# Optimization experiments

Measured on AMD Instinct MI355X. Metric: run time of the kernel, lower is better.

The kernel has to match this reference:

```python
import jax, jax.numpy as jnp
import numpy as np

M_USERS = 100000
N_ITEMS = 50000
N_NODES = M_USERS + N_ITEMS
DIM = 64
N_INTER = 1600000
BATCH = 16384
N_NEG = 40
REG = 1e-4


def setup_inputs() -> dict:
    key = jax.random.key(0)
    ks = jax.random.split(key, 12)
    xavier = lambda k, shape: jax.random.normal(k, shape, jnp.float32) * np.sqrt(2.0 / (shape[-1] + shape[-2] if len(shape) >= 2 else shape[-1] + 1))
    E = jax.random.normal(ks[0], (N_NODES, DIM), jnp.float32) * 0.1
    E2 = jax.random.normal(ks[1], (N_NODES, DIM), jnp.float32) * 0.1
    Wm = jax.random.normal(ks[2], (2, DIM, DIM), jnp.float32) * np.sqrt(1.0 / DIM)
    bm = jnp.zeros((2, DIM), jnp.float32)
    attn_W = jax.random.normal(ks[3], (DIM, DIM), jnp.float32) * np.sqrt(1.0 / DIM)
    attn_b = jnp.zeros((DIM,), jnp.float32)
    q_w = jax.random.normal(ks[4], (DIM,), jnp.float32) * np.sqrt(1.0 / DIM)
    # symmetric bipartite edge list: users in [0, M), items in [M, M+N)
    eu = jax.random.randint(ks[5], (N_INTER,), 0, M_USERS, jnp.int32)
    ei = jax.random.randint(ks[6], (N_INTER,), M_USERS, N_NODES, jnp.int32)
    edge_index = jnp.stack([jnp.concatenate([eu, ei]), jnp.concatenate([ei, eu])], axis=0)
    u = jax.random.randint(ks[7], (BATCH,), 0, M_USERS, jnp.int32)
    v = jax.random.randint(ks[8], (BATCH,), M_USERS, N_NODES, jnp.int32)
    n = jax.random.randint(ks[9], (BATCH, N_NEG), M_USERS, N_NODES, jnp.int32)
    w = jax.random.uniform(ks[10], (BATCH,), jnp.float32, 0.5, 5.0)  # ratings; only sign() used
    return {"E": E, "E2": E2, "Wm": Wm, "bm": bm, "attn_W": attn_W, "attn_b": attn_b,
            "q_w": q_w, "edge_index": edge_index, "u": u, "v": v, "n": n, "w": w}


def _lightgconv(x, src, dst, norm):
    # out[i] = sum_{(j->i)} norm_e * x[j]   (symmetric-normalized LightGCN propagate)
    msg = x[src] * norm[:, None]  # [E, D]
    return jax.ops.segment_sum(msg, dst, num_segments=N_NODES)


def _aggregate(E, E2, Wm, bm, attn_W, attn_b, q_w, edge_index):
    src, dst = edge_index[0], edge_index[1]
    deg = jax.ops.segment_sum(jnp.ones(src.shape, E.dtype), dst, num_segments=N_NODES)
    dinv = jnp.where(deg > 0, jax.lax.rsqrt(jnp.maximum(deg, 1.0)), 0.0)
    norm = dinv[src] * dinv[dst]
    # GNN branch: B = [E, conv(E), conv(conv(E))]; z_p = mean
    b1 = _lightgconv(E, src, dst, norm)
    b2 = _lightgconv(b1, src, dst, norm)
    z_p = (E + b1 + b2) / 3.0
    # MLP branch (eval mode: dropout disabled); z_n is output of last MLP layer
    x = jax.nn.relu(E2 @ Wm[0].T + bm[0])
    x = jax.nn.relu(x @ Wm[1].T + bm[1])
    z_n = x
    # attention fusion
    w_p = jnp.tanh(z_p @ attn_W.T + attn_b) @ q_w  # [Nn]
    w_n = jnp.tanh(z_n @ attn_W.T + attn_b) @ q_w  # [Nn]
    alpha = jax.nn.softmax(jnp.stack([w_p, w_n], axis=1), axis=1)  # [Nn, 2]
    return alpha[:, 0:1] * z_p + alpha[:, 1:2] * z_n


def reference(E, E2, Wm, bm, attn_W, attn_b, q_w, edge_index, u, v, n, w):
    Z = _aggregate(E, E2, Wm, bm, attn_W, attn_b, q_w, edge_index)
    u_ = Z[u]            # [B, D]
    v_ = Z[v]            # [B, D]
    n_ = Z[n]            # [B, K, D]
    pos = jnp.sum(u_ * v_, axis=1)                      # [B]
    neg = jnp.einsum('bd,bkd->bk', u_, n_)              # [B, K]
    sbpr = jax.nn.log_sigmoid(jnp.sign(w)[:, None] * pos[:, None] - neg).sum(axis=1)
    reg_loss = jnp.sum(u_ ** 2) + jnp.sum(v_ ** 2) + jnp.sum(n_ ** 2)
    return -jnp.sum(sbpr) + REG * reg_loss
```

## Files before the change

### kernel.cpp

```cpp
#include <hip/hip_runtime.h>
#include <math.h>


typedef unsigned int uint;
typedef unsigned short ushort;
typedef unsigned char uchar;
typedef unsigned long long ull;
typedef __attribute__((ext_vector_type(8))) short short8v;
typedef __attribute__((ext_vector_type(4))) float float4v;
typedef __attribute__((ext_vector_type(2))) float float2v;

#define BK_SHIFT 9
#define BK_SIZE 512
#define CAP 20480

#if __has_builtin(__builtin_amdgcn_cvt_pk_f32_fp8) && __has_builtin(__builtin_amdgcn_cvt_pk_fp8_f32)
#define HW_FP8 1
#else
#define HW_FP8 0
#endif

__device__ inline float b2f(ushort u) { return __uint_as_float(((uint)u) << 16); }
__device__ inline ushort f2b(float f) {
  uint u = __float_as_uint(f);
  return (ushort)((u + 0x7fffu + ((u >> 16) & 1u)) >> 16);
}
__device__ inline uint pack2(float lo, float hi) {
  return (uint)f2b(lo) | ((uint)f2b(hi) << 16);
}

__device__ inline float dec1(uint u) {
  uint e = (u >> 3) & 0xFu;
  uint m = u & 7u;
  uint s = (u & 0x80u) << 24;
  float norm = __uint_as_float(s | ((e + 120u) << 23) | (m << 20));
  float den = __uint_as_float(s | 0x3F800000u) * (float)(int)m * 0.001953125f;
  return e ? norm : den;
}
__device__ inline uint enc1(float x) {
  uint s = (__float_as_uint(x) >> 24) & 0x80u;
  float ax = fminf(fabsf(x), 448.f);
  uint r;
  if (ax < 0.015625f) {
    r = (uint)(int)rintf(ax * 512.f);
  } else {
    uint b = __float_as_uint(ax);
    b += 0x7FFFFu + ((b >> 20) & 1u);
    uint e = (b >> 23) - 120u;
    r = (e > 15u) ? 0x7Eu : ((e << 3) | ((b >> 20) & 7u));
  }
  return s | r;
}
__device__ inline float4 dec4(uint v) {
#if HW_FP8
  float2v lo = __builtin_amdgcn_cvt_pk_f32_fp8((int)v, false);
  float2v hi = __builtin_amdgcn_cvt_pk_f32_fp8((int)v, true);
  return make_float4(lo[0], lo[1], hi[0], hi[1]);
#else
  return make_float4(dec1(v & 0xFFu), dec1((v >> 8) & 0xFFu),
                     dec1((v >> 16) & 0xFFu), dec1(v >> 24));
#endif
}
__device__ inline uint enc4f(float a, float b, float c, float d) {
#if HW_FP8
  int v = 0;
  v = __builtin_amdgcn_cvt_pk_fp8_f32(a, b, v, false);
  v = __builtin_amdgcn_cvt_pk_fp8_f32(c, d, v, true);
  return (uint)v;
#else
  return enc1(a) | (enc1(b) << 8) | (enc1(c) << 16) | (enc1(d) << 24);
#endif
}

__global__ void k_half(const float* __restrict__ x, ushort* __restrict__ out, int n8) {
  int i = blockIdx.x * blockDim.x + threadIdx.x;
  if (i >= n8) return;
  const float4* p = (const float4*)(x + (size_t)i * 8);
  float4 a = p[0], b = p[1];
  uint4 o;
  o.x = pack2(a.x, a.y); o.y = pack2(a.z, a.w);
  o.z = pack2(b.x, b.y); o.w = pack2(b.z, b.w);
  ((uint4*)out)[i] = o;
}

__global__ void k_tofp8(const float* __restrict__ x, uint* __restrict__ out, int n16) {
  int i = blockIdx.x * blockDim.x + threadIdx.x;
  if (i >= n16) return;
  const float4* p = (const float4*)(x + (size_t)i * 16);
  float4 f0 = p[0], f1 = p[1], f2 = p[2], f3 = p[3];
  uint4 o;
  o.x = enc4f(f0.x, f0.y, f0.z, f0.w);
  o.y = enc4f(f1.x, f1.y, f1.z, f1.w);
  o.z = enc4f(f2.x, f2.y, f2.z, f2.w);
  o.w = enc4f(f3.x, f3.y, f3.z, f3.w);
  ((uint4*)out)[i] = o;
}

__global__ __launch_bounds__(512) void k_bucket(const int* __restrict__ src,
                                                const int* __restrict__ dst,
                                                int* __restrict__ gcursor,
                                                ull* __restrict__ ebuf,
                                                int NE, int nbkt, int chunk) {
  __shared__ int hist[1024];
  __shared__ int curb[1024];
  int tid = threadIdx.x;
  int nt = blockDim.x;
  for (int g = tid; g < nbkt; g += nt) hist[g] = 0;
  __syncthreads();
  int lo = blockIdx.x * chunk;
  int hi = min(lo + chunk, NE);
  for (int e = lo + tid; e < hi; e += nt)
    atomicAdd(&hist[dst[e] >> BK_SHIFT], 1);
  __syncthreads();
  for (int g = tid; g < nbkt; g += nt) {
    int c = hist[g];
    curb[g] = (c > 0) ? atomicAdd(&gcursor[g], c) : 0;
  }
  __syncthreads();
  for (int e = lo + tid; e < hi; e += nt) {
    int d = dst[e];
    int g = d >> BK_SHIFT;
    int pos = atomicAdd(&curb[g], 1);
    if (pos < CAP)
      ebuf[(size_t)g * CAP + pos] = ((ull)(uint)(d & (BK_SIZE - 1)) << 32) | (uint)src[e];
  }
}

__global__ void k_small(const int* __restrict__ gcursor, int* __restrict__ bktbase,
                        int nbkt) {
  __shared__ int sm[1024];
  int t = threadIdx.x;
  int v = (t < nbkt) ? gcursor[t] : 0;
  sm[t] = v;
  __syncthreads();
  for (int off = 1; off < 1024; off <<= 1) {
    int a = (t >= off) ? sm[t - off] : 0;
    __syncthreads();
    sm[t] += a;
    __syncthreads();
  }
  if (t < nbkt) bktbase[t] = sm[t] - v;
  if (t == 0) bktbase[nbkt] = sm[1023];
}

__global__ __launch_bounds__(256) void k_fine(const ull* __restrict__ ebuf,
                                              const int* __restrict__ gcursor,
                                              const int* __restrict__ bktbase,
                                              int* __restrict__ rowptr,
                                              float* __restrict__ dinv,
                                              int* __restrict__ csrc,
                                              int NN, int nbkt) {
  __shared__ int degl[BK_SIZE];
  __shared__ int lpl[BK_SIZE];
  __shared__ int ssum[256];
  int g = blockIdx.x;
  int tid = threadIdx.x;
  int cnt = gcursor[g];
  int base = bktbase[g];
  size_t ebase = (size_t)g * CAP;
  for (int j = tid; j < BK_SIZE; j += 256) degl[j] = 0;
  __syncthreads();
  for (int i = tid; i < cnt; i += 256)
    atomicAdd(&degl[(int)(ebuf[ebase + i] >> 32)], 1);
  __syncthreads();
  int d0 = degl[2 * tid], d1 = degl[2 * tid + 1];
  int s = d0 + d1;
  ssum[tid] = s;
  __syncthreads();
  for (int off = 1; off < 256; off <<= 1) {
    int a = (tid >= off) ? ssum[tid - off] : 0;
    __syncthreads();
    ssum[tid] += a;
    __syncthreads();
  }
  int excl = ssum[tid] - s;
  lpl[2 * tid] = excl;
  lpl[2 * tid + 1] = excl + d0;
  int node0 = g * BK_SIZE;
  int n0 = node0 + 2 * tid, n1 = n0 + 1;
  if (n0 < NN) {
    rowptr[n0] = base + excl;
    dinv[n0] = (d0 > 0) ? rsqrtf((float)d0) : 0.f;
  }
  if (n1 < NN) {
    rowptr[n1] = base + excl + d0;
    dinv[n1] = (d1 > 0) ? rsqrtf((float)d1) : 0.f;
  }
  if (g == nbkt - 1 && tid == 255) rowptr[NN] = base + excl + d0 + d1;
  __syncthreads();
  for (int i = tid; i < cnt; i += 256) {
    ull e = ebuf[ebase + i];
    int dl = (int)(e >> 32);
    int r = atomicAdd(&lpl[dl], 1);
    csrc[base + r] = (int)(uint)e;
  }
}

__global__ __launch_bounds__(256) void k_gather(const uint* __restrict__ x,
                                                const int* __restrict__ rowptr,
                                                const int* __restrict__ csrc,
                                                const float* __restrict__ dinv,
                                                uint* __restrict__ out, int NN) {
  int gid = blockIdx.x * blockDim.x + threadIdx.x;
  int node = gid >> 4;
  if (node >= NN) return;
  int sl = gid & 15;
  int beg = rowptr[node], end = rowptr[node + 1];
  float dn = dinv[node];
  float a0 = 0.f, a1 = 0.f, a2 = 0.f, a3 = 0.f;
  int i = beg;
  for (; i + 3 < end; i += 4) {
    int s0 = csrc[i], s1 = csrc[i + 1], s2 = csrc[i + 2], s3 = csrc[i + 3];
    float n0 = dinv[s0], n1 = dinv[s1], n2 = dinv[s2], n3 = dinv[s3];
    uint r0 = x[(size_t)s0 * 16 + sl];
    uint r1 = x[(size_t)s1 * 16 + sl];
    uint r2 = x[(size_t)s2 * 16 + sl];
    uint r3 = x[(size_t)s3 * 16 + sl];
    float4 d0 = dec4(r0), d1 = dec4(r1), d2 = dec4(r2), d3 = dec4(r3);
    a0 += n0 * d0.x; a1 += n0 * d0.y; a2 += n0 * d0.z; a3 += n0 * d0.w;
    a0 += n1 * d1.x; a1 += n1 * d1.y; a2 += n1 * d1.z; a3 += n1 * d1.w;
    a0 += n2 * d2.x; a1 += n2 * d2.y; a2 += n2 * d2.z; a3 += n2 * d2.w;
    a0 += n3 * d3.x; a1 += n3 * d3.y; a2 += n3 * d3.z; a3 += n3 * d3.w;
  }
  for (; i < end; ++i) {
    int s0 = csrc[i];
    float n0 = dinv[s0];
    float4 d0 = dec4(x[(size_t)s0 * 16 + sl]);
    a0 += n0 * d0.x; a1 += n0 * d0.y; a2 += n0 * d0.z; a3 += n0 * d0.w;
  }
  out[(size_t)node * 16 + sl] = enc4f(a0 * dn, a1 * dn, a2 * dn, a3 * dn);
}

__device__ inline float fast_tanh(float x) {
  float t = __expf(fminf(fmaxf(2.f * x, -30.f), 30.f));
  return (t - 1.f) / (t + 1.f);
}

__device__ inline short8v cvt8(const float* p) {
  float4 f0 = *(const float4*)p;
  float4 f1 = *(const float4*)(p + 4);
  uint4 u;
  u.x = pack2(f0.x, f0.y); u.y = pack2(f0.z, f0.w);
  u.z = pack2(f1.x, f1.y); u.w = pack2(f1.z, f1.w);
  return *(short8v*)&u;
}

#define MFMA(a, b, c) __builtin_amdgcn_mfma_f32_16x16x32_bf16((a), (b), (c), 0, 0, 0)

__global__ __launch_bounds__(256, 2) void k_node(const float* __restrict__ E,
                                                 const float* __restrict__ E2,
                                                 const ushort* __restrict__ Wmh,
                                                 const float* __restrict__ bm,
                                                 const ushort* __restrict__ AWh,
                                                 const float* __restrict__ ab,
                                                 const float* __restrict__ qw,
                                                 const uint* __restrict__ b1q,
                                                 const uint* __restrict__ b2q,
                                                 float* __restrict__ Zf,
                                                 int NN) {
  __shared__ ushort Hl[64 * 72];
  __shared__ ushort Pl[64 * 72];
  int tid = threadIdx.x;
  int lane = tid & 63, wid = tid >> 6;
  int r15 = lane & 15, kg = lane >> 4;
  int node0 = blockIdx.x * 64;

  int arow = node0 + 16 * wid + r15;
  int arowc = min(arow, NN - 1);
  const float* e2p = E2 + (size_t)arowc * 64 + 8 * kg;
  short8v a0 = cvt8(e2p);
  short8v a1 = cvt8(e2p + 32);
  float4v acc[4];
#pragma unroll
  for (int b = 0; b < 4; ++b) {
    int col = r15 + 16 * b;
    short8v w0 = *(const short8v*)&Wmh[col * 64 + 8 * kg];
    short8v w1 = *(const short8v*)&Wmh[col * 64 + 32 + 8 * kg];
    float bias = bm[col];
    acc[b] = (float4v){bias, bias, bias, bias};
    acc[b] = MFMA(a0, w0, acc[b]);
    acc[b] = MFMA(a1, w1, acc[b]);
  }
#pragma unroll
  for (int b = 0; b < 4; ++b)
#pragma unroll
    for (int rr = 0; rr < 4; ++rr)
      Hl[(16 * wid + 4 * kg + rr) * 72 + 16 * b + r15] = f2b(fmaxf(acc[b][rr], 0.f));

  {
    int row = tid >> 2;
    int c4 = (tid & 3) * 4;
    int node = node0 + row;
    uint outp[8];
    if (node < NN) {
      const float* pe = E + (size_t)node * 64 + c4 * 4;
      uint4 q1 = *(const uint4*)(b1q + (size_t)node * 16 + c4);
      uint4 q2 = *(const uint4*)(b2q + (size_t)node * 16 + c4);
      float4 d1[4] = {dec4(q1.x), dec4(q1.y), dec4(q1.z), dec4(q1.w)};
      float4 d2[4] = {dec4(q2.x), dec4(q2.y), dec4(q2.z), dec4(q2.w)};
#pragma unroll
      for (int c = 0; c < 4; ++c) {
        float4 e4 = ((const float4*)pe)[c];
        float z0 = (e4.x + d1[c].x + d2[c].x) * (1.f / 3.f);
        float z1 = (e4.y + d1[c].y + d2[c].y) * (1.f / 3.f);
        float z2 = (e4.z + d1[c].z + d2[c].z) * (1.f / 3.f);
        float z3 = (e4.w + d1[c].w + d2[c].w) * (1.f / 3.f);
        outp[2 * c] = pack2(z0, z1);
        outp[2 * c + 1] = pack2(z2, z3);
      }
    } else {
#pragma unroll
      for (int c = 0; c < 8; ++c) outp[c] = 0;
    }
    int c0 = c4 * 4;
    *(uint4*)&Pl[row * 72 + c0] = *(uint4*)&outp[0];
    *(uint4*)&Pl[row * 72 + c0 + 8] = *(uint4*)&outp[4];
  }
  __syncthreads();

  const ushort* hap = &Hl[(16 * wid + r15) * 72 + 8 * kg];
  short8v ha0 = *(const short8v*)hap;
  short8v ha1 = *(const short8v*)(hap + 32);
  float4v acc2[4];
#pragma unroll
  for (int b = 0; b < 4; ++b) {
    int col = r15 + 16 * b;
    short8v w0 = *(const short8v*)&Wmh[4096 + col * 64 + 8 * kg];
    short8v w1 = *(const short8v*)&Wmh[4096 + col * 64 + 32 + 8 * kg];
    float bias = bm[64 + col];
    acc2[b] = (float4v){bias, bias, bias, bias};
    acc2[b] = MFMA(ha0, w0, acc2[b]);
    acc2[b] = MFMA(ha1, w1, acc2[b]);
  }
  __syncthreads();
#pragma unroll
  for (int b = 0; b < 4; ++b)
#pragma unroll
    for (int rr = 0; rr < 4; ++rr)
      Hl[(16 * wid + 4 * kg + rr) * 72 + 16 * b + r15] = f2b(fmaxf(acc2[b][rr], 0.f));
  __syncthreads();

  const ushort* pap = &Pl[(16 * wid + r15) * 72 + 8 * kg];
  short8v pa0 = *(const short8v*)pap;
  short8v pa1 = *(const short8v*)(pap + 32);
  const ushort* nap = &Hl[(16 * wid + r15) * 72 + 8 * kg];
  short8v na0 = *(const short8v*)nap;
  short8v na1 = *(const short8v*)(nap + 32);
  float4v ac1[4], ac2[4];
#pragma unroll
  for (int b = 0; b < 4; ++b) {
    int col = r15 + 16 * b;
    short8v w0 = *(const short8v*)&AWh[col * 64 + 8 * kg];
    short8v w1 = *(const short8v*)&AWh[col * 64 + 32 + 8 * kg];
    float bias = ab[col];
    ac1[b] = (float4v){bias, bias, bias, bias};
    ac1[b] = MFMA(pa0, w0, ac1[b]);
    ac1[b] = MFMA(pa1, w1, ac1[b]);
    ac2[b] = (float4v){bias, bias, bias, bias};
    ac2[b] = MFMA(na0, w0, ac2[b]);
    ac2[b] = MFMA(na1, w1, ac2[b]);
  }

  float qv[4];
#pragma unroll
  for (int b = 0; b < 4; ++b) qv[b] = qw[r15 + 16 * b];
#pragma unroll
  for (int rr = 0; rr < 4; ++rr) {
    float wp = 0.f, wn = 0.f;
#pragma unroll
    for (int b = 0; b < 4; ++b) {
      wp += fast_tanh(ac1[b][rr]) * qv[b];
      wn += fast_tanh(ac2[b][rr]) * qv[b];
    }
#pragma unroll
    for (int off = 8; off; off >>= 1) {
      wp += __shfl_xor(wp, off);
      wn += __shfl_xor(wn, off);
    }
    float m = fmaxf(wp, wn);
    float e1 = __expf(wp - m), e2 = __expf(wn - m);
    float inv = 1.f / (e1 + e2);
    float al0 = e1 * inv, al1 = e2 * inv;
    int row_l = 16 * wid + 4 * kg + rr;
    int node = node0 + row_l;
    if (node < NN) {
      float* op = Zf + (size_t)node * 64;
#pragma unroll
      for (int b = 0; b < 4; ++b) {
        int col = r15 + 16 * b;
        int li = row_l * 72 + col;
        op[col] = al0 * b2f(Pl[li]) + al1 * b2f(Hl[li]);
      }
    }
  }
}

__global__ __launch_bounds__(256) void k_score(const float* __restrict__ Z,
                                               const int* __restrict__ u,
                                               const int* __restrict__ v,
                                               const int* __restrict__ n,
                                               const float* __restrict__ w,
                                               float* __restrict__ out, int B, int K) {
  __shared__ float xbuf[16][65];
  __shared__ float part[16];
  int t = threadIdx.x;
  int wv = t >> 6, lane = t & 63;
  int sg = lane >> 4, sl = lane & 15;
  int bloc = wv * 4 + sg;
  int b = blockIdx.x * 16 + bloc;
  float lossb = 0.f;
  if (b < B) {
    int uid = u[b], vid = v[b];
    float4 u4 = *(const float4*)&Z[(size_t)uid * 64 + sl * 4];
    float4 v4 = *(const float4*)&Z[(size_t)vid * 64 + sl * 4];
    float p = u4.x * v4.x + u4.y * v4.y + u4.z * v4.z + u4.w * v4.w;
#pragma unroll
    for (int off = 8; off; off >>= 1) p += __shfl_xor(p, off);
    float wb = w[b];
    float sgn = (wb > 0.f) ? 1.f : ((wb < 0.f) ? -1.f : 0.f);
    float sp = sgn * p;
    float regl = u4.x * u4.x + u4.y * u4.y + u4.z * u4.z + u4.w * u4.w
               + v4.x * v4.x + v4.y * v4.y + v4.z * v4.z + v4.w * v4.w;
    const int* nb_ = n + (size_t)b * K;
    for (int k = 0; k < K; ++k) {
      int nid = nb_[k];
      float4 n4 = *(const float4*)&Z[(size_t)nid * 64 + sl * 4];
      float d = u4.x * n4.x + u4.y * n4.y + u4.z * n4.z + u4.w * n4.w;
      regl += n4.x * n4.x + n4.y * n4.y + n4.z * n4.z + n4.w * n4.w;
#pragma unroll
      for (int off = 8; off; off >>= 1) d += __shfl_xor(d, off);
      if (sl == 0) xbuf[bloc][k] = sp - d;
    }
#pragma unroll
    for (int off = 8; off; off >>= 1) regl += __shfl_xor(regl, off);
    float sb = 0.f;
    for (int k = sl; k < K; k += 16) {
      float x = xbuf[bloc][k];
      sb += fminf(x, 0.f) - log1pf(expf(-fabsf(x)));
    }
#pragma unroll
    for (int off = 8; off; off >>= 1) sb += __shfl_xor(sb, off);
    lossb = -sb + 1e-4f * regl;
  }
  if (sl == 0) part[bloc] = (b < B) ? lossb : 0.f;
  __syncthreads();
  if (t == 0) {
    float s = 0.f;
#pragma unroll
    for (int i = 0; i < 16; ++i) s += part[i];
    unsafeAtomicAdd(out, s);
  }
}

extern "C" void kernel_launch(void* const* d_in, const int* in_sizes, int n_in,
                              void* d_out, int out_size, void* d_ws, size_t ws_size,
                              hipStream_t stream) {
  const float* E  = (const float*)d_in[0];
  const float* E2 = (const float*)d_in[1];
  const float* Wm = (const float*)d_in[2];
  const float* bm = (const float*)d_in[3];
  const float* AW = (const float*)d_in[4];
  const float* ab = (const float*)d_in[5];
  const float* qw = (const float*)d_in[6];
  const int*   ei = (const int*)d_in[7];
  const int*   u  = (const int*)d_in[8];
  const int*   v  = (const int*)d_in[9];
  const int*   nn = (const int*)d_in[10];
  const float* w  = (const float*)d_in[11];

  const int NN = in_sizes[0] / 64;
  const int NE = in_sizes[7] / 2;
  const int B  = in_sizes[8];
  const int K  = in_sizes[10] / B;
  const int NBKT = (NN + BK_SIZE - 1) / BK_SIZE;

  const int* src = ei;
  const int* dst = ei + NE;

  float*  ws      = (float*)d_ws;
  float*  dinv    = ws;
  uint*   E8      = (uint*)(dinv + NN);
  uint*   b1q     = E8 + (size_t)NN * 16;
  uint*   b2q     = b1q + (size_t)NN * 16;
  ushort* Wmh     = (ushort*)(b2q + (size_t)NN * 16);
  ushort* AWh     = Wmh + 8192;
  int*    rowptr  = (int*)(AWh + 4096);
  int*    csrc    = rowptr + NN + 1;
  int*    gcursor = csrc + NE;
  int*    bktbase = gcursor + NBKT;
  ull*    ebuf    = (ull*)(((uintptr_t)(bktbase + NBKT + 1) + 15) & ~(uintptr_t)15);
  float*  Zf      = (float*)ebuf;
  float*  outf    = (float*)d_out;

  hipMemsetAsync(gcursor, 0, (size_t)NBKT * sizeof(int), stream);
  hipMemsetAsync(outf, 0, sizeof(float), stream);

  k_tofp8<<<(NN * 4 + 255) / 256, 256, 0, stream>>>(E, E8, NN * 4);
  k_half<<<4, 256, 0, stream>>>(Wm, Wmh, 1024);
  k_half<<<2, 256, 0, stream>>>(AW, AWh, 512);

  const int BUCKET_BLOCKS = 512;
  int chunk = (NE + BUCKET_BLOCKS - 1) / BUCKET_BLOCKS;
  k_bucket<<<BUCKET_BLOCKS, 512, 0, stream>>>(src, dst, gcursor, ebuf, NE, NBKT, chunk);
  k_small<<<1, 1024, 0, stream>>>(gcursor, bktbase, NBKT);
  k_fine<<<NBKT, 256, 0, stream>>>(ebuf, gcursor, bktbase, rowptr, dinv, csrc, NN, NBKT);

  int gatherBlocks = ((size_t)NN * 16 + 255) / 256;
  k_gather<<<gatherBlocks, 256, 0, stream>>>(E8, rowptr, csrc, dinv, b1q, NN);
  k_gather<<<gatherBlocks, 256, 0, stream>>>(b1q, rowptr, csrc, dinv, b2q, NN);

  int nodeTiles = (NN + 63) / 64;
  k_node<<<nodeTiles, 256, 0, stream>>>(E, E2, Wmh, bm, AWh, ab, qw, b1q, b2q, Zf, NN);

  k_score<<<(B + 15) / 16, 256, 0, stream>>>(Zf, u, v, nn, w, outf, B, K);
}
```

Before: 294.1 us.

## Store fused embeddings in bf16, pre-convert E/E2, unroll gather by eight

The final fused embedding Z is now written and read as bf16 instead of fp32. This halves the bytes moved by the random-access negative-sampling score kernel and by the node kernel's output. E and E2 are converted to bf16 in separate passes before the gathers, so the node kernel reads half-width inputs. The CSR gather loop is unrolled to eight edges with a second accumulator set to expose more memory-level parallelism. The extra conversion passes add their own full read and write of E2 and E, and bf16 Z lowers the precision of the loss.

```diff
diff --git a/kernel.cpp b/kernel.cpp
--- a/kernel.cpp
+++ b/kernel.cpp
@@ -4,7 +4,6 @@
 
 typedef unsigned int uint;
 typedef unsigned short ushort;
-typedef unsigned char uchar;
 typedef unsigned long long ull;
 typedef __attribute__((ext_vector_type(8))) short short8v;
 typedef __attribute__((ext_vector_type(4))) float float4v;
@@ -83,17 +82,25 @@
   ((uint4*)out)[i] = o;
 }
 
-__global__ void k_tofp8(const float* __restrict__ x, uint* __restrict__ out, int n16) {
+__global__ void k_conv_e(const float* __restrict__ x, uint* __restrict__ out8,
+                         ushort* __restrict__ outh, int n16) {
   int i = blockIdx.x * blockDim.x + threadIdx.x;
   if (i >= n16) return;
   const float4* p = (const float4*)(x + (size_t)i * 16);
   float4 f0 = p[0], f1 = p[1], f2 = p[2], f3 = p[3];
-  uint4 o;
-  o.x = enc4f(f0.x, f0.y, f0.z, f0.w);
-  o.y = enc4f(f1.x, f1.y, f1.z, f1.w);
-  o.z = enc4f(f2.x, f2.y, f2.z, f2.w);
-  o.w = enc4f(f3.x, f3.y, f3.z, f3.w);
-  ((uint4*)out)[i] = o;
+  uint4 o8;
+  o8.x = enc4f(f0.x, f0.y, f0.z, f0.w);
+  o8.y = enc4f(f1.x, f1.y, f1.z, f1.w);
+  o8.z = enc4f(f2.x, f2.y, f2.z, f2.w);
+  o8.w = enc4f(f3.x, f3.y, f3.z, f3.w);
+  ((uint4*)out8)[i] = o8;
+  uint4 h0, h1;
+  h0.x = pack2(f0.x, f0.y); h0.y = pack2(f0.z, f0.w);
+  h0.z = pack2(f1.x, f1.y); h0.w = pack2(f1.z, f1.w);
+  h1.x = pack2(f2.x, f2.y); h1.y = pack2(f2.z, f2.w);
+  h1.z = pack2(f3.x, f3.y); h1.w = pack2(f3.z, f3.w);
+  ((uint4*)outh)[2 * i] = h0;
+  ((uint4*)outh)[2 * i + 1] = h1;
 }
 
 __global__ __launch_bounds__(512) void k_bucket(const int* __restrict__ src,
@@ -208,19 +215,31 @@
   int beg = rowptr[node], end = rowptr[node + 1];
   float dn = dinv[node];
   float a0 = 0.f, a1 = 0.f, a2 = 0.f, a3 = 0.f;
+  float b0 = 0.f, b1 = 0.f, b2 = 0.f, b3 = 0.f;
   int i = beg;
-  for (; i + 3 < end; i += 4) {
+  for (; i + 7 < end; i += 8) {
     int s0 = csrc[i], s1 = csrc[i + 1], s2 = csrc[i + 2], s3 = csrc[i + 3];
+    int s4 = csrc[i + 4], s5 = csrc[i + 5], s6 = csrc[i + 6], s7 = csrc[i + 7];
     float n0 = dinv[s0], n1 = dinv[s1], n2 = dinv[s2], n3 = dinv[s3];
+    float n4 = dinv[s4], n5 = dinv[s5], n6 = dinv[s6], n7 = dinv[s7];
     uint r0 = x[(size_t)s0 * 16 + sl];
     uint r1 = x[(size_t)s1 * 16 + sl];
     uint r2 = x[(size_t)s2 * 16 + sl];
     uint r3 = x[(size_t)s3 * 16 + sl];
+    uint r4 = x[(size_t)s4 * 16 + sl];
+    uint r5 = x[(size_t)s5 * 16 + sl];
+    uint r6 = x[(size_t)s6 * 16 + sl];
+    uint r7 = x[(size_t)s7 * 16 + sl];
     float4 d0 = dec4(r0), d1 = dec4(r1), d2 = dec4(r2), d3 = dec4(r3);
+    float4 d4 = dec4(r4), d5 = dec4(r5), d6 = dec4(r6), d7 = dec4(r7);
     a0 += n0 * d0.x; a1 += n0 * d0.y; a2 += n0 * d0.z; a3 += n0 * d0.w;
     a0 += n1 * d1.x; a1 += n1 * d1.y; a2 += n1 * d1.z; a3 += n1 * d1.w;
     a0 += n2 * d2.x; a1 += n2 * d2.y; a2 += n2 * d2.z; a3 += n2 * d2.w;
     a0 += n3 * d3.x; a1 += n3 * d3.y; a2 += n3 * d3.z; a3 += n3 * d3.w;
+    b0 += n4 * d4.x; b1 += n4 * d4.y; b2 += n4 * d4.z; b3 += n4 * d4.w;
+    b0 += n5 * d5.x; b1 += n5 * d5.y; b2 += n5 * d5.z; b3 += n5 * d5.w;
+    b0 += n6 * d6.x; b1 += n6 * d6.y; b2 += n6 * d6.z; b3 += n6 * d6.w;
+    b0 += n7 * d7.x; b1 += n7 * d7.y; b2 += n7 * d7.z; b3 += n7 * d7.w;
   }
   for (; i < end; ++i) {
     int s0 = csrc[i];
@@ -228,6 +247,7 @@
     float4 d0 = dec4(x[(size_t)s0 * 16 + sl]);
     a0 += n0 * d0.x; a1 += n0 * d0.y; a2 += n0 * d0.z; a3 += n0 * d0.w;
   }
+  a0 += b0; a1 += b1; a2 += b2; a3 += b3;
   out[(size_t)node * 16 + sl] = enc4f(a0 * dn, a1 * dn, a2 * dn, a3 * dn);
 }
 
@@ -236,19 +256,10 @@
   return (t - 1.f) / (t + 1.f);
 }
 
-__device__ inline short8v cvt8(const float* p) {
-  float4 f0 = *(const float4*)p;
-  float4 f1 = *(const float4*)(p + 4);
-  uint4 u;
-  u.x = pack2(f0.x, f0.y); u.y = pack2(f0.z, f0.w);
-  u.z = pack2(f1.x, f1.y); u.w = pack2(f1.z, f1.w);
-  return *(short8v*)&u;
-}
-
 #define MFMA(a, b, c) __builtin_amdgcn_mfma_f32_16x16x32_bf16((a), (b), (c), 0, 0, 0)
 
-__global__ __launch_bounds__(256, 2) void k_node(const float* __restrict__ E,
-                                                 const float* __restrict__ E2,
+__global__ __launch_bounds__(256, 2) void k_node(const ushort* __restrict__ Ebf,
+                                                 const ushort* __restrict__ E2h,
                                                  const ushort* __restrict__ Wmh,
                                                  const float* __restrict__ bm,
                                                  const ushort* __restrict__ AWh,
@@ -256,7 +267,7 @@
                                                  const float* __restrict__ qw,
                                                  const uint* __restrict__ b1q,
                                                  const uint* __restrict__ b2q,
-                                                 float* __restrict__ Zf,
+                                                 ushort* __restrict__ Zh,
                                                  int NN) {
   __shared__ ushort Hl[64 * 72];
   __shared__ ushort Pl[64 * 72];
@@ -267,9 +278,9 @@
 
   int arow = node0 + 16 * wid + r15;
   int arowc = min(arow, NN - 1);
-  const float* e2p = E2 + (size_t)arowc * 64 + 8 * kg;
-  short8v a0 = cvt8(e2p);
-  short8v a1 = cvt8(e2p + 32);
+  const ushort* e2p = E2h + (size_t)arowc * 64 + 8 * kg;
+  short8v a0 = *(const short8v*)e2p;
+  short8v a1 = *(const short8v*)(e2p + 32);
   float4v acc[4];
 #pragma unroll
   for (int b = 0; b < 4; ++b) {
@@ -293,18 +304,26 @@
     int node = node0 + row;
     uint outp[8];
     if (node < NN) {
-      const float* pe = E + (size_t)node * 64 + c4 * 4;
+      const ushort* pe = Ebf + (size_t)node * 64 + c4 * 4;
+      uint4 eh0 = *(const uint4*)pe;
+      uint4 eh1 = *(const uint4*)(pe + 8);
       uint4 q1 = *(const uint4*)(b1q + (size_t)node * 16 + c4);
       uint4 q2 = *(const uint4*)(b2q + (size_t)node * 16 + c4);
       float4 d1[4] = {dec4(q1.x), dec4(q1.y), dec4(q1.z), dec4(q1.w)};
       float4 d2[4] = {dec4(q2.x), dec4(q2.y), dec4(q2.z), dec4(q2.w)};
+      const uint* ehw = (const uint*)&eh0;
+      uint ehall[8] = {eh0.x, eh0.y, eh0.z, eh0.w, eh1.x, eh1.y, eh1.z, eh1.w};
+      (void)ehw;
 #pragma unroll
       for (int c = 0; c < 4; ++c) {
-        float4 e4 = ((const float4*)pe)[c];
-        float z0 = (e4.x + d1[c].x + d2[c].x) * (1.f / 3.f);
-        float z1 = (e4.y + d1[c].y + d2[c].y) * (1.f / 3.f);
-        float z2 = (e4.z + d1[c].z + d2[c].z) * (1.f / 3.f);
-        float z3 = (e4.w + d1[c].w + d2[c].w) * (1.f / 3.f);
+        float e0 = b2f((ushort)(ehall[2 * c] & 0xFFFFu));
+        float e1 = b2f((ushort)(ehall[2 * c] >> 16));
+        float e2 = b2f((ushort)(ehall[2 * c + 1] & 0xFFFFu));
+        float e3 = b2f((ushort)(ehall[2 * c + 1] >> 16));
+        float z0 = (e0 + d1[c].x + d2[c].x) * (1.f / 3.f);
+        float z1 = (e1 + d1[c].y + d2[c].y) * (1.f / 3.f);
+        float z2 = (e2 + d1[c].z + d2[c].z) * (1.f / 3.f);
+        float z3 = (e3 + d1[c].w + d2[c].w) * (1.f / 3.f);
         outp[2 * c] = pack2(z0, z1);
         outp[2 * c + 1] = pack2(z2, z3);
       }
@@ -384,18 +403,18 @@
     int row_l = 16 * wid + 4 * kg + rr;
     int node = node0 + row_l;
     if (node < NN) {
-      float* op = Zf + (size_t)node * 64;
+      ushort* op = Zh + (size_t)node * 64;
 #pragma unroll
       for (int b = 0; b < 4; ++b) {
         int col = r15 + 16 * b;
         int li = row_l * 72 + col;
-        op[col] = al0 * b2f(Pl[li]) + al1 * b2f(Hl[li]);
+        op[col] = f2b(al0 * b2f(Pl[li]) + al1 * b2f(Hl[li]));
       }
     }
   }
 }
 
-__global__ __launch_bounds__(256) void k_score(const float* __restrict__ Z,
+__global__ __launch_bounds__(256) void k_score(const ushort* __restrict__ Z,
                                                const int* __restrict__ u,
                                                const int* __restrict__ v,
                                                const int* __restrict__ n,
@@ -411,22 +430,25 @@
   float lossb = 0.f;
   if (b < B) {
     int uid = u[b], vid = v[b];
-    float4 u4 = *(const float4*)&Z[(size_t)uid * 64 + sl * 4];
-    float4 v4 = *(const float4*)&Z[(size_t)vid * 64 + sl * 4];
-    float p = u4.x * v4.x + u4.y * v4.y + u4.z * v4.z + u4.w * v4.w;
+    ushort4 uh = *(const ushort4*)&Z[(size_t)uid * 64 + sl * 4];
+    ushort4 vh = *(const ushort4*)&Z[(size_t)vid * 64 + sl * 4];
+    float ux = b2f(uh.x), uy = b2f(uh.y), uz = b2f(uh.z), uw = b2f(uh.w);
+    float vx = b2f(vh.x), vy = b2f(vh.y), vz = b2f(vh.z), vw = b2f(vh.w);
+    float p = ux * vx + uy * vy + uz * vz + uw * vw;
 #pragma unroll
     for (int off = 8; off; off >>= 1) p += __shfl_xor(p, off);
     float wb = w[b];
     float sgn = (wb > 0.f) ? 1.f : ((wb < 0.f) ? -1.f : 0.f);
     float sp = sgn * p;
-    float regl = u4.x * u4.x + u4.y * u4.y + u4.z * u4.z + u4.w * u4.w
-               + v4.x * v4.x + v4.y * v4.y + v4.z * v4.z + v4.w * v4.w;
+    float regl = ux * ux + uy * uy + uz * uz + uw * uw
+               + vx * vx + vy * vy + vz * vz + vw * vw;
     const int* nb_ = n + (size_t)b * K;
     for (int k = 0; k < K; ++k) {
       int nid = nb_[k];
-      float4 n4 = *(const float4*)&Z[(size_t)nid * 64 + sl * 4];
-      float d = u4.x * n4.x + u4.y * n4.y + u4.z * n4.z + u4.w * n4.w;
-      regl += n4.x * n4.x + n4.y * n4.y + n4.z * n4.z + n4.w * n4.w;
+      ushort4 nh = *(const ushort4*)&Z[(size_t)nid * 64 + sl * 4];
+      float nx = b2f(nh.x), ny = b2f(nh.y), nz = b2f(nh.z), nw = b2f(nh.w);
+      float d = ux * nx + uy * ny + uz * nz + uw * nw;
+      regl += nx * nx + ny * ny + nz * nz + nw * nw;
 #pragma unroll
       for (int off = 8; off; off >>= 1) d += __shfl_xor(d, off);
       if (sl == 0) xbuf[bloc][k] = sp - d;
@@ -482,22 +504,20 @@
   uint*   E8      = (uint*)(dinv + NN);
   uint*   b1q     = E8 + (size_t)NN * 16;
   uint*   b2q     = b1q + (size_t)NN * 16;
-  ushort* Wmh     = (ushort*)(b2q + (size_t)NN * 16);
+  ushort* E2h     = (ushort*)(b2q + (size_t)NN * 16);
+  ushort* Wmh     = E2h + (size_t)NN * 64;
   ushort* AWh     = Wmh + 8192;
   int*    rowptr  = (int*)(AWh + 4096);
   int*    csrc    = rowptr + NN + 1;
   int*    gcursor = csrc + NE;
   int*    bktbase = gcursor + NBKT;
   ull*    ebuf    = (ull*)(((uintptr_t)(bktbase + NBKT + 1) + 15) & ~(uintptr_t)15);
-  float*  Zf      = (float*)ebuf;
+  ushort* Zh      = (ushort*)ebuf;
+  ushort* Ebf     = Zh + (size_t)NN * 64;
   float*  outf    = (float*)d_out;
 
   hipMemsetAsync(gcursor, 0, (size_t)NBKT * sizeof(int), stream);
   hipMemsetAsync(outf, 0, sizeof(float), stream);
-
-  k_tofp8<<<(NN * 4 + 255) / 256, 256, 0, stream>>>(E, E8, NN * 4);
-  k_half<<<4, 256, 0, stream>>>(Wm, Wmh, 1024);
-  k_half<<<2, 256, 0, stream>>>(AW, AWh, 512);
 
   const int BUCKET_BLOCKS = 512;
   int chunk = (NE + BUCKET_BLOCKS - 1) / BUCKET_BLOCKS;
@@ -505,12 +525,17 @@
   k_small<<<1, 1024, 0, stream>>>(gcursor, bktbase, NBKT);
   k_fine<<<NBKT, 256, 0, stream>>>(ebuf, gcursor, bktbase, rowptr, dinv, csrc, NN, NBKT);
 
+  k_conv_e<<<(NN * 4 + 255) / 256, 256, 0, stream>>>(E, E8, Ebf, NN * 4);
+  k_half<<<(NN * 8 + 255) / 256, 256, 0, stream>>>(E2, E2h, NN * 8);
+  k_half<<<4, 256, 0, stream>>>(Wm, Wmh, 1024);
+  k_half<<<2, 256, 0, stream>>>(AW, AWh, 512);
+
   int gatherBlocks = ((size_t)NN * 16 + 255) / 256;
   k_gather<<<gatherBlocks, 256, 0, stream>>>(E8, rowptr, csrc, dinv, b1q, NN);
   k_gather<<<gatherBlocks, 256, 0, stream>>>(b1q, rowptr, csrc, dinv, b2q, NN);
 
   int nodeTiles = (NN + 63) / 64;
-  k_node<<<nodeTiles, 256, 0, stream>>>(E, E2, Wmh, bm, AWh, ab, qw, b1q, b2q, Zf, NN);
-
-  k_score<<<(B + 15) / 16, 256, 0, stream>>>(Zf, u, v, nn, w, outf, B, K);
-}
+  k_node<<<nodeTiles, 256, 0, stream>>>(Ebf, E2h, Wmh, bm, AWh, ab, qw, b1q, b2q, Zh, NN);
+
+  k_score<<<(B + 15) / 16, 256, 0, stream>>>(Zh, u, v, nn, w, outf, B, K);
+}
```

Result: slower. 303.6 us (+3.2%).
